# Kernel optimization log

Measured on AMD Instinct MI355X. Metric: run time of the kernel, lower is better.

## Reference

```python
import jax, jax.numpy as jnp
import numpy as np

FEAT = 3136          # conved_channel//8 * pooled_size**2 = 512//8 * 7*7
HIDDEN = 64
NUM_CLASSES = 21
SELECTED_PROPOSAL = 128
LEAKY_SLOPE = 0.1


def leaky_relu(x, slope=LEAKY_SLOPE):
    return jnp.where(x >= 0, x, slope * x)


def setup_inputs() -> dict:
    key = jax.random.key(0)
    k_x, k_kc, k_w1, k_b1, k_w2, k_b2 = jax.random.split(key, 6)
    B, R = 64, 300
    x = jax.random.normal(k_x, (B, R, FEAT), dtype=jnp.float32)
    keep_count = jax.random.randint(k_kc, (B,), 0, R, dtype=jnp.int32)
    # nn.Linear default init: U(-1/sqrt(fan_in), 1/sqrt(fan_in))
    bnd1 = 1.0 / np.sqrt(FEAT)
    W1 = jax.random.uniform(k_w1, (FEAT, HIDDEN), jnp.float32, -bnd1, bnd1)
    b1 = jax.random.uniform(k_b1, (HIDDEN,), jnp.float32, -bnd1, bnd1)
    bnd2 = 1.0 / np.sqrt(HIDDEN)
    W2 = jax.random.uniform(k_w2, (HIDDEN, NUM_CLASSES), jnp.float32, -bnd2, bnd2)
    b2 = jax.random.uniform(k_b2, (NUM_CLASSES,), jnp.float32, -bnd2, bnd2)
    return {"x": x, "W1": W1, "b1": b1, "W2": W2, "b2": b2, "keep_count": keep_count}


def reference(x, W1, b1, W2, b2, keep_count):
    # x: [B, R, FEAT]; only the first SELECTED_PROPOSAL ROIs can be written.
    B = x.shape[0]
    S = SELECTED_PROPOSAL
    xs = x.reshape(B, x.shape[1], -1)[:, :S, :]                 # [B, S, F]
    h = leaky_relu(jnp.einsum('bsf,fh->bsh', xs, W1) + b1)      # [B, S, 64]
    # Dropout(0.25) is identity in eval mode.
    out = leaky_relu(jnp.einsum('bsh,hk->bsk', h, W2) + b2)     # [B, S, K]
    # rows j >= min(keep_count[idx], S) stay zero
    limit = jnp.minimum(keep_count, S)                          # [B]
    mask = jnp.arange(S)[None, :] < limit[:, None]              # [B, S]
    return jnp.where(mask[:, :, None], out, jnp.zeros((), out.dtype))
```

## Files before the change

### kernel.cpp

```cpp
#include <hip/hip_runtime.h>
#include <hip/hip_bf16.h>

static constexpr int FEAT_  = 3136;
static constexpr int KSTEPS = 98;
static constexpr int RSTR   = 300;
static constexpr int SROWS  = 128;
static constexpr int HID    = 64;
static constexpr int NCLS   = 21;
static constexpr int BM     = 32;

typedef __attribute__((ext_vector_type(8))) short bf16x8;
typedef __attribute__((ext_vector_type(4))) float f32x4;

__device__ bf16x8 g_w1p[KSTEPS * 4 * 64];

__device__ __forceinline__ short f2bf(float f) {
    union { float f; unsigned u; } v; v.f = f;
    unsigned r = v.u + 0x7fffu + ((v.u >> 16) & 1u);
    return (short)(r >> 16);
}

__global__ __launch_bounds__(256) void pack_w1(const float* __restrict__ W1) {
    int t = blockIdx.x * 256 + threadIdx.x;
    int lane = t & 63;
    int nt   = (t >> 6) & 3;
    int ks   = t >> 8;
    int col  = nt * 16 + (lane & 15);
    int g    = lane >> 4;
    int k0   = ks * 32 + g * 4;
    bf16x8 v;
    #pragma unroll
    for (int j = 0; j < 4; ++j) v[j]     = f2bf(W1[(k0 + j) * HID + col]);
    #pragma unroll
    for (int j = 0; j < 4; ++j) v[4 + j] = f2bf(W1[(k0 + 16 + j) * HID + col]);
    g_w1p[t] = v;
}

__global__ __launch_bounds__(512) void fused_main(
    const float* __restrict__ x,  const float* __restrict__ b1,
    const float* __restrict__ W2, const float* __restrict__ b2,
    const int*  __restrict__ keep, float* __restrict__ out)
{
    const int tid  = threadIdx.x;
    const int lane = tid & 63;
    const int wv   = tid >> 6;
    const int row_base = blockIdx.x * BM;
    const int b      = row_base >> 7;
    const int s_base = row_base & 127;

    float* outp = out + row_base * NCLS;
    const int limit = min(keep[b], SROWS);

    if (s_base >= limit) {
        for (int i = tid; i < BM * NCLS; i += 512) outp[i] = 0.f;
        return;
    }

    __shared__ float hp[8][BM][HID + 1];
    __shared__ float hf[BM][HID + 2];
    __shared__ float w2s[HID * NCLS];

    for (int i = tid; i < HID * NCLS; i += 512) w2s[i] = W2[i];

    const int ks0 = (wv * KSTEPS) >> 3;
    const int ks1 = ((wv + 1) * KSTEPS) >> 3;

    const int g = lane >> 4;
    const int r = lane & 15;
    const int row0 = min(s_base + r,      limit - 1);
    const int row1 = min(s_base + 16 + r, limit - 1);
    const float* xp0 = x + (b * RSTR + row0) * FEAT_ + g * 4;
    const float* xp1 = x + (b * RSTR + row1) * FEAT_ + g * 4;
    const bf16x8* wp = g_w1p + lane;

    f32x4 a00 = {0,0,0,0}, a01 = {0,0,0,0}, a02 = {0,0,0,0}, a03 = {0,0,0,0};
    f32x4 a10 = {0,0,0,0}, a11 = {0,0,0,0}, a12 = {0,0,0,0}, a13 = {0,0,0,0};

    #pragma unroll 2
    for (int ks = ks0; ks < ks1; ++ks) {
        float4 p0a = *(const float4*)(xp0 + ks * 32);
        float4 p0b = *(const float4*)(xp0 + ks * 32 + 16);
        float4 p1a = *(const float4*)(xp1 + ks * 32);
        float4 p1b = *(const float4*)(xp1 + ks * 32 + 16);
        bf16x8 bv0 = wp[(ks * 4 + 0) * 64];
        bf16x8 bv1 = wp[(ks * 4 + 1) * 64];
        bf16x8 bv2 = wp[(ks * 4 + 2) * 64];
        bf16x8 bv3 = wp[(ks * 4 + 3) * 64];
        bf16x8 af0, af1;
        af0[0]=f2bf(p0a.x); af0[1]=f2bf(p0a.y); af0[2]=f2bf(p0a.z); af0[3]=f2bf(p0a.w);
        af0[4]=f2bf(p0b.x); af0[5]=f2bf(p0b.y); af0[6]=f2bf(p0b.z); af0[7]=f2bf(p0b.w);
        af1[0]=f2bf(p1a.x); af1[1]=f2bf(p1a.y); af1[2]=f2bf(p1a.z); af1[3]=f2bf(p1a.w);
        af1[4]=f2bf(p1b.x); af1[5]=f2bf(p1b.y); af1[6]=f2bf(p1b.z); af1[7]=f2bf(p1b.w);
        a00 = __builtin_amdgcn_mfma_f32_16x16x32_bf16(af0, bv0, a00, 0, 0, 0);
        a01 = __builtin_amdgcn_mfma_f32_16x16x32_bf16(af0, bv1, a01, 0, 0, 0);
        a02 = __builtin_amdgcn_mfma_f32_16x16x32_bf16(af0, bv2, a02, 0, 0, 0);
        a03 = __builtin_amdgcn_mfma_f32_16x16x32_bf16(af0, bv3, a03, 0, 0, 0);
        a10 = __builtin_amdgcn_mfma_f32_16x16x32_bf16(af1, bv0, a10, 0, 0, 0);
        a11 = __builtin_amdgcn_mfma_f32_16x16x32_bf16(af1, bv1, a11, 0, 0, 0);
        a12 = __builtin_amdgcn_mfma_f32_16x16x32_bf16(af1, bv2, a12, 0, 0, 0);
        a13 = __builtin_amdgcn_mfma_f32_16x16x32_bf16(af1, bv3, a13, 0, 0, 0);
    }

    #pragma unroll
    for (int rr = 0; rr < 4; ++rr) {
        const int mr0 = g * 4 + rr, mr1 = 16 + g * 4 + rr;
        hp[wv][mr0][r     ] = a00[rr];
        hp[wv][mr0][r + 16] = a01[rr];
        hp[wv][mr0][r + 32] = a02[rr];
        hp[wv][mr0][r + 48] = a03[rr];
        hp[wv][mr1][r     ] = a10[rr];
        hp[wv][mr1][r + 16] = a11[rr];
        hp[wv][mr1][r + 32] = a12[rr];
        hp[wv][mr1][r + 48] = a13[rr];
    }
    __syncthreads();

    for (int e = tid; e < BM * HID; e += 512) {
        int row = e >> 6, col = e & 63;
        float v = b1[col];
        #pragma unroll
        for (int p = 0; p < 8; ++p) v += hp[p][row][col];
        hf[row][col] = (v >= 0.f) ? v : 0.1f * v;
    }
    __syncthreads();

    for (int idx = tid; idx < BM * NCLS; idx += 512) {
        int rI = idx / NCLS;
        int c  = idx - rI * NCLS;
        float a2 = b2[c];
        #pragma unroll 8
        for (int col = 0; col < HID; ++col)
            a2 += hf[rI][col] * w2s[col * NCLS + c];
        a2 = (a2 >= 0.f) ? a2 : 0.1f * a2;
        outp[idx] = (s_base + rI < limit) ? a2 : 0.f;
    }
}

extern "C" void kernel_launch(void* const* d_in, const int* in_sizes, int n_in,
                              void* d_out, int out_size, void* d_ws, size_t ws_size,
                              hipStream_t stream) {
    const float* x    = (const float*)d_in[0];
    const float* W1   = (const float*)d_in[1];
    const float* b1   = (const float*)d_in[2];
    const float* W2   = (const float*)d_in[3];
    const float* b2   = (const float*)d_in[4];
    const int*   keep = (const int*)d_in[5];
    float* out = (float*)d_out;

    hipLaunchKernelGGL(pack_w1,    dim3(KSTEPS), dim3(256), 0, stream, W1);
    hipLaunchKernelGGL(fused_main, dim3((64 * SROWS) / BM), dim3(512), 0, stream,
                       x, b1, W2, b2, keep, out);
}
```

Before: 29.03 us.

## Merge weight packing into main kernel with global atomic flag handoff

Folds the W1 bf16 packing kernel into the main kernel: the first 32 blocks pack the weights and bump a global counter, and compute blocks spin on that counter before their MFMA loop. This removes one kernel launch and the gap between the two kernels, and lets the main blocks set up their addresses while packing is still running. The last block to finish resets the counters for the next call. The spin-wait relies on the packing blocks being scheduled alongside the waiting blocks, which holds here since the grid fits on the device, and waiting blocks may stall while packing completes.

```diff
diff --git a/kernel.cpp b/kernel.cpp
--- a/kernel.cpp
+++ b/kernel.cpp
@@ -8,11 +8,16 @@
 static constexpr int HID    = 64;
 static constexpr int NCLS   = 21;
 static constexpr int BM     = 32;
+static constexpr int PACKB  = 32;
+static constexpr int NFRAG  = KSTEPS * 4 * 64;
+static constexpr int MAINB  = (64 * SROWS) / BM;
 
 typedef __attribute__((ext_vector_type(8))) short bf16x8;
 typedef __attribute__((ext_vector_type(4))) float f32x4;
 
-__device__ bf16x8 g_w1p[KSTEPS * 4 * 64];
+__device__ bf16x8 g_w1p[NFRAG];
+__device__ int g_done;
+__device__ int g_main_done;
 
 __device__ __forceinline__ short f2bf(float f) {
     union { float f; unsigned u; } v; v.f = f;
@@ -20,31 +25,39 @@
     return (short)(r >> 16);
 }
 
-__global__ __launch_bounds__(256) void pack_w1(const float* __restrict__ W1) {
-    int t = blockIdx.x * 256 + threadIdx.x;
-    int lane = t & 63;
-    int nt   = (t >> 6) & 3;
-    int ks   = t >> 8;
-    int col  = nt * 16 + (lane & 15);
-    int g    = lane >> 4;
-    int k0   = ks * 32 + g * 4;
-    bf16x8 v;
-    #pragma unroll
-    for (int j = 0; j < 4; ++j) v[j]     = f2bf(W1[(k0 + j) * HID + col]);
-    #pragma unroll
-    for (int j = 0; j < 4; ++j) v[4 + j] = f2bf(W1[(k0 + 16 + j) * HID + col]);
-    g_w1p[t] = v;
-}
+__global__ __launch_bounds__(512, 2) void fused_all(
+    const float* __restrict__ x,  const float* __restrict__ W1,
+    const float* __restrict__ b1, const float* __restrict__ W2,
+    const float* __restrict__ b2, const int* __restrict__ keep,
+    float* __restrict__ out)
+{
+    const int tid = threadIdx.x;
 
-__global__ __launch_bounds__(512) void fused_main(
-    const float* __restrict__ x,  const float* __restrict__ b1,
-    const float* __restrict__ W2, const float* __restrict__ b2,
-    const int*  __restrict__ keep, float* __restrict__ out)
-{
-    const int tid  = threadIdx.x;
+    if (blockIdx.x < PACKB) {
+        for (int t = blockIdx.x * 512 + tid; t < NFRAG; t += PACKB * 512) {
+            int lane = t & 63;
+            int nt   = (t >> 6) & 3;
+            int ks   = t >> 8;
+            int col  = nt * 16 + (lane & 15);
+            int g    = lane >> 4;
+            int k0   = ks * 32 + g * 4;
+            bf16x8 v;
+            #pragma unroll
+            for (int j = 0; j < 4; ++j) v[j]     = f2bf(W1[(k0 + j) * HID + col]);
+            #pragma unroll
+            for (int j = 0; j < 4; ++j) v[4 + j] = f2bf(W1[(k0 + 16 + j) * HID + col]);
+            g_w1p[t] = v;
+        }
+        __threadfence();
+        __syncthreads();
+        if (tid == 0) atomicAdd(&g_done, 1);
+        return;
+    }
+
+    const int bid  = blockIdx.x - PACKB;
     const int lane = tid & 63;
     const int wv   = tid >> 6;
-    const int row_base = blockIdx.x * BM;
+    const int row_base = bid * BM;
     const int b      = row_base >> 7;
     const int s_base = row_base & 127;
 
@@ -53,6 +66,14 @@
 
     if (s_base >= limit) {
         for (int i = tid; i < BM * NCLS; i += 512) outp[i] = 0.f;
+        __syncthreads();
+        if (tid == 0) {
+            int n = atomicAdd(&g_main_done, 1);
+            if (n == MAINB - 1) {
+                __hip_atomic_store(&g_main_done, 0, __ATOMIC_RELAXED, __HIP_MEMORY_SCOPE_AGENT);
+                __hip_atomic_store(&g_done, 0, __ATOMIC_RELAXED, __HIP_MEMORY_SCOPE_AGENT);
+            }
+        }
         return;
     }
 
@@ -72,6 +93,13 @@
     const float* xp0 = x + (b * RSTR + row0) * FEAT_ + g * 4;
     const float* xp1 = x + (b * RSTR + row1) * FEAT_ + g * 4;
     const bf16x8* wp = g_w1p + lane;
+
+    if (tid == 0) {
+        while (__hip_atomic_load(&g_done, __ATOMIC_ACQUIRE, __HIP_MEMORY_SCOPE_AGENT) < PACKB)
+            __builtin_amdgcn_s_sleep(4);
+        __threadfence();
+    }
+    __syncthreads();
 
     f32x4 a00 = {0,0,0,0}, a01 = {0,0,0,0}, a02 = {0,0,0,0}, a03 = {0,0,0,0};
     f32x4 a10 = {0,0,0,0}, a11 = {0,0,0,0}, a12 = {0,0,0,0}, a13 = {0,0,0,0};
@@ -134,6 +162,15 @@
         a2 = (a2 >= 0.f) ? a2 : 0.1f * a2;
         outp[idx] = (s_base + rI < limit) ? a2 : 0.f;
     }
+
+    __syncthreads();
+    if (tid == 0) {
+        int n = atomicAdd(&g_main_done, 1);
+        if (n == MAINB - 1) {
+            __hip_atomic_store(&g_main_done, 0, __ATOMIC_RELAXED, __HIP_MEMORY_SCOPE_AGENT);
+            __hip_atomic_store(&g_done, 0, __ATOMIC_RELAXED, __HIP_MEMORY_SCOPE_AGENT);
+        }
+    }
 }
 
 extern "C" void kernel_launch(void* const* d_in, const int* in_sizes, int n_in,
@@ -147,7 +184,6 @@
     const int*   keep = (const int*)d_in[5];
     float* out = (float*)d_out;
 
-    hipLaunchKernelGGL(pack_w1,    dim3(KSTEPS), dim3(256), 0, stream, W1);
-    hipLaunchKernelGGL(fused_main, dim3((64 * SROWS) / BM), dim3(512), 0, stream,
-                       x, b1, W2, b2, keep, out);
+    hipLaunchKernelGGL(fused_all, dim3(PACKB + MAINB), dim3(512), 0, stream,
+                       x, W1, b1, W2, b2, keep, out);
 }
```

Result: slower. 61.93 us (+113.4%).
